# Performance work log

Hardware: AMD Instinct MI355X
Metric: run time of the kernel (lower is better)

The kernel has to match this reference:

```python
import jax, jax.numpy as jnp
import numpy as np

K = 20  # rec list length

def _isin(a, b, bmask=None):
    # membership of each element of a in (masked) b; a,b are small [K] int arrays
    eq = a[:, None] == b[None, :]
    if bmask is not None:
        eq = eq & bmask[None, :]
    return eq.any(axis=1)

def _compact(vals, mask):
    # stable compaction of masked elements to the front, preserving order
    n = vals.shape[0]
    order = jnp.argsort(jnp.where(mask, jnp.arange(n), n))
    return vals[order], mask.sum()

def _fuse_one(top, mid, sim, probs, key):
    # greedy set-intersection fusion of three K-length rec lists (mirrors __fuse_rec_lists)
    m_tm = _isin(top, mid)
    m_ts = _isin(top, sim)
    m_ms = _isin(mid, sim)
    # faithful to the torch code's elementwise AND of masks over different lists
    mask_common = m_tm & m_ts & m_ms
    in_common_mid = _isin(mid, top, mask_common)
    mask_tm = m_tm & ~mask_common
    mask_ts = m_ts & ~mask_common
    mask_ms = m_ms & ~in_common_mid
    top_pool_m = ~mask_common & ~mask_tm & ~mask_ts
    mid_pool_m = ~in_common_mid & ~_isin(mid, top, mask_tm) & ~mask_ms
    sim_pool_m = (~_isin(sim, top, mask_common) & ~_isin(sim, top, mask_ts)
                  & ~_isin(sim, mid, mask_ms))
    det_vals = jnp.concatenate([top, top, top, mid])          # [4K]
    det_mask = jnp.concatenate([mask_common, mask_tm, mask_ts, mask_ms])
    det, n_det = _compact(det_vals, det_mask)
    pools, counts = jax.vmap(_compact)(
        jnp.stack([top, mid, sim]),
        jnp.stack([top_pool_m, mid_pool_m, sim_pool_m]))      # [3,K], [3]
    logp = jnp.log(probs)

    def step(carry, t):
        ptr, key = carry
        key, sub = jax.random.split(key)
        avail = ptr < counts
        idx = jax.random.categorical(sub, jnp.where(avail, logp, -jnp.inf))
        sampled = pools[idx, jnp.minimum(ptr[idx], K - 1)]
        use_det = t < n_det
        val = jnp.where(use_det, det[t], sampled)
        ptr = ptr.at[idx].add(jnp.where(use_det, 0, 1))
        return (ptr, key), val

    _, out = jax.lax.scan(step, (jnp.zeros(3, jnp.int32), key), jnp.arange(K))
    return out

def setup_inputs() -> dict:
    key = jax.random.key(0)
    ks = jax.random.split(key, 9)
    B, p_dim, latent = 2048, 64, 128
    n_users, n_items = 2000, 20000
    n_top, n_mid = 2000, 5000
    rng = np.random.default_rng(0)
    perm = rng.permutation(n_items)
    return {
        "X": jax.random.normal(ks[0], (B, p_dim), jnp.float32),
        "W_sp": jax.random.normal(ks[1], (p_dim, latent), jnp.float32) * 0.1,
        "W_sd": jax.random.normal(ks[2], (latent, n_top), jnp.float32) * 0.1,
        "W_mp": jax.random.normal(ks[3], (p_dim, latent), jnp.float32) * 0.1,
        "W_md": jax.random.normal(ks[4], (latent, n_mid), jnp.float32) * 0.1,
        "W_mapper": jax.random.normal(ks[5], (p_dim, 3), jnp.float32) * 0.1,
        "user_ratings": jax.random.uniform(ks[6], (n_users, n_items), jnp.float32),
        "user_personalities": jax.random.normal(ks[7], (n_users, p_dim), jnp.float32),
        "top_map": jnp.asarray(perm[:n_top], jnp.int32),
        "mid_map": jnp.asarray(perm[n_top:n_top + n_mid], jnp.int32),
    }

def reference(X, W_sp, W_sd, W_mp, W_md, W_mapper, user_ratings,
              user_personalities, top_map, mid_map):
    B = X.shape[0]
    n_items = user_ratings.shape[1]
    # small decoder path: prior -> dec -> scatter into full item space
    top_sub = (X @ W_sp) @ W_sd                                  # [B, n_top]
    top_full = jnp.zeros((B, n_items), X.dtype).at[:, top_map].set(top_sub)
    mid_sub = (X @ W_mp) @ W_md                                  # [B, n_mid]
    mid_full = jnp.zeros((B, n_items), X.dtype).at[:, mid_map].set(mid_sub)
    # personality-similarity recommendations
    sim_scores = (X @ user_personalities.T) @ user_ratings       # [B, n_items]
    top_idx = jax.lax.top_k(top_full, K)[1].astype(jnp.int32)
    mid_idx = jax.lax.top_k(mid_full, K)[1].astype(jnp.int32)
    sim_idx = jax.lax.top_k(sim_scores, K)[1].astype(jnp.int32)
    probs = jax.nn.softmax(X @ W_mapper, axis=-1)                # [B, 3]
    keys = jax.random.split(jax.random.key(42), B)
    out = jax.vmap(_fuse_one)(top_idx, mid_idx, sim_idx, probs, keys)
    return out.astype(jnp.float32)                               # [B, K]
```

## Files before the change

kernel.cpp:

```cpp
#include <hip/hip_runtime.h>
#include <stdint.h>
#include <math.h>

#define KK 20
#define RNG_PARTITIONABLE 1


__device__ __forceinline__ void tf2x32(uint32_t k0, uint32_t k1,
                                       uint32_t c0, uint32_t c1,
                                       uint32_t& o0, uint32_t& o1) {
  const uint32_t ks2 = k0 ^ k1 ^ 0x1BD11BDAu;
  uint32_t x0 = c0 + k0, x1 = c1 + k1;
#define ROTL32(x,d) (((x) << (d)) | ((x) >> (32 - (d))))
#define R4(ra,rb,rc,rd) \
  x0 += x1; x1 = ROTL32(x1, ra); x1 ^= x0; \
  x0 += x1; x1 = ROTL32(x1, rb); x1 ^= x0; \
  x0 += x1; x1 = ROTL32(x1, rc); x1 ^= x0; \
  x0 += x1; x1 = ROTL32(x1, rd); x1 ^= x0;
  R4(13,15,26,6);  x0 += k1;  x1 += ks2 + 1u;
  R4(17,29,16,24); x0 += ks2; x1 += k0 + 2u;
  R4(13,15,26,6);  x0 += k0;  x1 += k1 + 3u;
  R4(17,29,16,24); x0 += k1;  x1 += ks2 + 4u;
  R4(13,15,26,6);  x0 += ks2; x1 += k0 + 5u;
  o0 = x0; o1 = x1;
#undef R4
#undef ROTL32
}

__device__ __forceinline__ float u01_from_bits(uint32_t b) {
  float f = __uint_as_float((b >> 9) | 0x3f800000u) - 1.0f;
  return (f == 0.0f) ? 1.17549435e-38f : f;
}

#define BK 32

__global__ __launch_bounds__(256) void gemm_nn_k(
    const float* __restrict__ A, int lda,
    const float* __restrict__ Bg, int ldb,
    float* __restrict__ C, int ldc,
    int M, int N, int K, int kc) {
  __shared__ __align__(16) float As[BK][64 + 4];
  __shared__ __align__(16) float Bs[BK][128 + 4];
  const int tid = threadIdx.x;
  const int row0 = blockIdx.y * 64;
  const int col0 = blockIdx.x * 128;
  const int tr = tid >> 4, tc = tid & 15;
  const int kc_eff = (kc > 0) ? kc : K;

  const int a_ar0 = tid >> 3,        a_ac0 = (tid & 7) << 2;
  const int a_ar1 = (tid + 256) >> 3, a_ac1 = ((tid + 256) & 7) << 2;
  int b_br[4], b_bc[4];
#pragma unroll
  for (int i = 0; i < 4; ++i) { int s = tid + i * 256; b_br[i] = s >> 5; b_bc[i] = (s & 31) << 2; }

  float4 pa0, pa1, pb[4];
  auto load_tile = [&](int k0) {
    {
      int gr = row0 + a_ar0, gc = k0 + a_ac0;
      float4 v = make_float4(0.f, 0.f, 0.f, 0.f);
      if (gr < M) {
        if (gc + 3 < K) v = *(const float4*)(A + (size_t)gr * lda + gc);
        else {
          float t0 = (gc     < K) ? A[(size_t)gr * lda + gc]     : 0.f;
          float t1 = (gc + 1 < K) ? A[(size_t)gr * lda + gc + 1] : 0.f;
          float t2 = (gc + 2 < K) ? A[(size_t)gr * lda + gc + 2] : 0.f;
          float t3 = (gc + 3 < K) ? A[(size_t)gr * lda + gc + 3] : 0.f;
          v = make_float4(t0, t1, t2, t3);
        }
      }
      pa0 = v;
    }
    {
      int gr = row0 + a_ar1, gc = k0 + a_ac1;
      float4 v = make_float4(0.f, 0.f, 0.f, 0.f);
      if (gr < M) {
        if (gc + 3 < K) v = *(const float4*)(A + (size_t)gr * lda + gc);
        else {
          float t0 = (gc     < K) ? A[(size_t)gr * lda + gc]     : 0.f;
          float t1 = (gc + 1 < K) ? A[(size_t)gr * lda + gc + 1] : 0.f;
          float t2 = (gc + 2 < K) ? A[(size_t)gr * lda + gc + 2] : 0.f;
          float t3 = (gc + 3 < K) ? A[(size_t)gr * lda + gc + 3] : 0.f;
          v = make_float4(t0, t1, t2, t3);
        }
      }
      pa1 = v;
    }
#pragma unroll
    for (int i = 0; i < 4; ++i) {
      int gk = k0 + b_br[i], gc = col0 + b_bc[i];
      float4 v = make_float4(0.f, 0.f, 0.f, 0.f);
      if (gk < K) {
        if (gc + 3 < N) v = *(const float4*)(Bg + (size_t)gk * ldb + gc);
        else {
          float t0 = (gc     < N) ? Bg[(size_t)gk * ldb + gc]     : 0.f;
          float t1 = (gc + 1 < N) ? Bg[(size_t)gk * ldb + gc + 1] : 0.f;
          float t2 = (gc + 2 < N) ? Bg[(size_t)gk * ldb + gc + 2] : 0.f;
          float t3 = (gc + 3 < N) ? Bg[(size_t)gk * ldb + gc + 3] : 0.f;
          v = make_float4(t0, t1, t2, t3);
        }
      }
      pb[i] = v;
    }
  };

  float accM[4][8];
#pragma unroll
  for (int i = 0; i < 4; ++i)
#pragma unroll
    for (int j = 0; j < 8; ++j) accM[i][j] = 0.f;

  for (int c0 = 0; c0 < K; c0 += kc_eff) {
    const int kend = (c0 + kc_eff < K) ? (c0 + kc_eff) : K;
    float acc[4][8];
#pragma unroll
    for (int i = 0; i < 4; ++i)
#pragma unroll
      for (int j = 0; j < 8; ++j) acc[i][j] = 0.f;

    load_tile(c0);
    for (int k0 = c0; k0 < kend; k0 += BK) {
      As[a_ac0 + 0][a_ar0] = pa0.x; As[a_ac0 + 1][a_ar0] = pa0.y;
      As[a_ac0 + 2][a_ar0] = pa0.z; As[a_ac0 + 3][a_ar0] = pa0.w;
      As[a_ac1 + 0][a_ar1] = pa1.x; As[a_ac1 + 1][a_ar1] = pa1.y;
      As[a_ac1 + 2][a_ar1] = pa1.z; As[a_ac1 + 3][a_ar1] = pa1.w;
#pragma unroll
      for (int i = 0; i < 4; ++i) *(float4*)&Bs[b_br[i]][b_bc[i]] = pb[i];
      __syncthreads();
      if (k0 + BK < kend) load_tile(k0 + BK);
      const int klim = (kend - k0 < BK) ? (kend - k0) : BK;
      for (int kk = 0; kk < klim; ++kk) {
        float4 av = *(const float4*)&As[kk][tr << 2];
        float4 b0 = *(const float4*)&Bs[kk][tc << 2];
        float4 b1 = *(const float4*)&Bs[kk][64 + (tc << 2)];
        float a[4] = {av.x, av.y, av.z, av.w};
        float b[8] = {b0.x, b0.y, b0.z, b0.w, b1.x, b1.y, b1.z, b1.w};
#pragma unroll
        for (int i = 0; i < 4; ++i)
#pragma unroll
          for (int j = 0; j < 8; ++j)
            acc[i][j] = __fadd_rn(acc[i][j], __fmul_rn(a[i], b[j]));
      }
      __syncthreads();
    }
#pragma unroll
    for (int i = 0; i < 4; ++i)
#pragma unroll
      for (int j = 0; j < 8; ++j) accM[i][j] = __fadd_rn(accM[i][j], acc[i][j]);
  }
#pragma unroll
  for (int i = 0; i < 4; ++i) {
    int gr = row0 + (tr << 2) + i;
    if (gr >= M) continue;
#pragma unroll
    for (int j = 0; j < 8; ++j) {
      int gc = col0 + ((j < 4) ? (tc << 2) + j : 64 + (tc << 2) + (j - 4));
      if (gc < N) C[(size_t)gr * ldc + gc] = accM[i][j];
    }
  }
}

__global__ __launch_bounds__(256) void gemm_nt_k(
    const float* __restrict__ A, int lda,
    const float* __restrict__ Bg, int ldb,
    float* __restrict__ C, int ldc,
    int M, int N, int K) {
  __shared__ __align__(16) float As[16][128 + 4];
  __shared__ __align__(16) float Bs[16][128 + 4];
  const int tid = threadIdx.x;
  const int row0 = blockIdx.y * 128;
  const int col0 = blockIdx.x * 128;
  const int tr = tid >> 4, tc = tid & 15;
  float acc[8][8];
#pragma unroll
  for (int i = 0; i < 8; ++i)
#pragma unroll
    for (int j = 0; j < 8; ++j) acc[i][j] = 0.f;

  for (int k0 = 0; k0 < K; k0 += 16) {
#pragma unroll
    for (int i = 0; i < 2; ++i) {
      int s = tid + i * 256;
      int ar = s >> 2, ac = (s & 3) << 2;
      int gr = row0 + ar, gc = k0 + ac;
      float4 v = make_float4(0.f, 0.f, 0.f, 0.f);
      if (gr < M) {
        if (gc + 3 < K) v = *(const float4*)(A + (size_t)gr * lda + gc);
        else {
          float t0 = (gc     < K) ? A[(size_t)gr * lda + gc]     : 0.f;
          float t1 = (gc + 1 < K) ? A[(size_t)gr * lda + gc + 1] : 0.f;
          float t2 = (gc + 2 < K) ? A[(size_t)gr * lda + gc + 2] : 0.f;
          float t3 = (gc + 3 < K) ? A[(size_t)gr * lda + gc + 3] : 0.f;
          v = make_float4(t0, t1, t2, t3);
        }
      }
      As[ac + 0][ar] = v.x; As[ac + 1][ar] = v.y;
      As[ac + 2][ar] = v.z; As[ac + 3][ar] = v.w;
    }
#pragma unroll
    for (int i = 0; i < 2; ++i) {
      int s = tid + i * 256;
      int nr = s >> 2, kcc = (s & 3) << 2;
      int gn = col0 + nr, gk = k0 + kcc;
      float4 v = make_float4(0.f, 0.f, 0.f, 0.f);
      if (gn < N) {
        if (gk + 3 < K) v = *(const float4*)(Bg + (size_t)gn * ldb + gk);
        else {
          float t0 = (gk     < K) ? Bg[(size_t)gn * ldb + gk]     : 0.f;
          float t1 = (gk + 1 < K) ? Bg[(size_t)gn * ldb + gk + 1] : 0.f;
          float t2 = (gk + 2 < K) ? Bg[(size_t)gn * ldb + gk + 2] : 0.f;
          float t3 = (gk + 3 < K) ? Bg[(size_t)gn * ldb + gk + 3] : 0.f;
          v = make_float4(t0, t1, t2, t3);
        }
      }
      Bs[kcc + 0][nr] = v.x; Bs[kcc + 1][nr] = v.y;
      Bs[kcc + 2][nr] = v.z; Bs[kcc + 3][nr] = v.w;
    }
    __syncthreads();
#pragma unroll
    for (int kk = 0; kk < 16; ++kk) {
      float4 a0 = *(const float4*)&As[kk][tr * 8];
      float4 a1 = *(const float4*)&As[kk][tr * 8 + 4];
      float4 b0 = *(const float4*)&Bs[kk][tc * 8];
      float4 b1 = *(const float4*)&Bs[kk][tc * 8 + 4];
      float a[8] = {a0.x, a0.y, a0.z, a0.w, a1.x, a1.y, a1.z, a1.w};
      float b[8] = {b0.x, b0.y, b0.z, b0.w, b1.x, b1.y, b1.z, b1.w};
#pragma unroll
      for (int i = 0; i < 8; ++i)
#pragma unroll
        for (int j = 0; j < 8; ++j)
          acc[i][j] = __fadd_rn(acc[i][j], __fmul_rn(a[i], b[j]));
    }
    __syncthreads();
  }
#pragma unroll
  for (int i = 0; i < 8; ++i) {
    int gr = row0 + tr * 8 + i;
    if (gr >= M) continue;
#pragma unroll
    for (int j = 0; j < 8; ++j) {
      int gc = col0 + tc * 8 + j;
      if (gc < N) C[(size_t)gr * ldc + gc] = acc[i][j];
    }
  }
}

__device__ __forceinline__ void topk20_row(
    const float* __restrict__ row, int ncols, int col_off,
    const int* __restrict__ map,
    float* __restrict__ SV, int* __restrict__ SI, int merge,
    float (*shv)[KK], int (*shi)[KK], float* ov, int* oi) {
  const int t = threadIdx.x;
  float lv[KK]; int li[KK];
#pragma unroll
  for (int i = 0; i < KK; ++i) { lv[i] = -INFINITY; li[i] = 0x7fffffff; }
  for (int c = t; c < ncols; c += 256) {
    float v = row[c];
    if (v > lv[KK - 1]) {
      float cv = v; int ci = c;
#pragma unroll
      for (int i = 0; i < KK; ++i) {
        bool sw = cv > lv[i];
        float tv = lv[i]; int ti = li[i];
        lv[i] = sw ? cv : tv; li[i] = sw ? ci : ti;
        cv = sw ? tv : cv;    ci = sw ? ti : ci;
      }
    }
  }
#pragma unroll
  for (int i = 0; i < KK; ++i) { shv[t][i] = lv[i]; shi[t][i] = li[i]; }
  __syncthreads();
  if (t < 64) {
    int hp0 = 0, hp1 = 0, hp2 = 0, hp3 = 0;
    for (int round = 0; round < KK; ++round) {
      int base = t * 4;
      float v0 = (hp0 < KK) ? shv[base + 0][hp0] : -INFINITY;
      int   i0 = (hp0 < KK) ? shi[base + 0][hp0] : 0x7fffffff;
      float v1 = (hp1 < KK) ? shv[base + 1][hp1] : -INFINITY;
      int   i1 = (hp1 < KK) ? shi[base + 1][hp1] : 0x7fffffff;
      float v2 = (hp2 < KK) ? shv[base + 2][hp2] : -INFINITY;
      int   i2 = (hp2 < KK) ? shi[base + 2][hp2] : 0x7fffffff;
      float v3 = (hp3 < KK) ? shv[base + 3][hp3] : -INFINITY;
      int   i3 = (hp3 < KK) ? shi[base + 3][hp3] : 0x7fffffff;
      float bv = v0; int bi = i0; int bq = 0;
      if (v1 > bv || (v1 == bv && i1 < bi)) { bv = v1; bi = i1; bq = 1; }
      if (v2 > bv || (v2 == bv && i2 < bi)) { bv = v2; bi = i2; bq = 2; }
      if (v3 > bv || (v3 == bv && i3 < bi)) { bv = v3; bi = i3; bq = 3; }
      float cv = bv; int ci = bi; int cl = t; int cq = bq;
#pragma unroll
      for (int s2 = 1; s2 < 64; s2 <<= 1) {
        float vx = __shfl_xor(cv, s2);
        int   ix = __shfl_xor(ci, s2);
        int   lx = __shfl_xor(cl, s2);
        int   qx = __shfl_xor(cq, s2);
        if (vx > cv || (vx == cv && ix < ci)) { cv = vx; ci = ix; cl = lx; cq = qx; }
      }
      if (t == 0) { ov[round] = cv; oi[round] = ci; }
      if (cl == t) { hp0 += (cq == 0); hp1 += (cq == 1); hp2 += (cq == 2); hp3 += (cq == 3); }
    }
    if (t == 0) {
      if (!merge) {
        for (int i = 0; i < KK; ++i) {
          SV[i] = ov[i];
          SI[i] = map ? map[oi[i]] : (oi[i] + col_off);
        }
      } else {
        float mv[KK]; int mi[KK];
        int a = 0, b = 0;
        for (int i = 0; i < KK; ++i) {
          float va = SV[a]; int ia = SI[a];
          float vb = ov[b]; int ib = oi[b] + col_off;
          bool ta = (va > vb) || (va == vb && ia < ib);
          if (ta) { mv[i] = va; mi[i] = ia; ++a; }
          else    { mv[i] = vb; mi[i] = ib; ++b; }
        }
        for (int i = 0; i < KK; ++i) { SV[i] = mv[i]; SI[i] = mi[i]; }
      }
    }
  }
}

__global__ __launch_bounds__(256) void topk20_k(
    const float* __restrict__ mat, int ld, int ncols, int col_off,
    const int* __restrict__ map,
    float* __restrict__ sval, int* __restrict__ sidx, int merge) {
  __shared__ float shv[256][KK];
  __shared__ int   shi[256][KK];
  __shared__ float ov[KK];
  __shared__ int   oi[KK];
  const int r = blockIdx.x;
  topk20_row(mat + (size_t)r * ld, ncols, col_off, map,
             sval + (size_t)r * KK, sidx + (size_t)r * KK, merge, shv, shi, ov, oi);
}

__global__ __launch_bounds__(256) void topk20_dual_k(
    const float* __restrict__ m0, int nc0, const int* __restrict__ map0,
    float* __restrict__ sv0, int* __restrict__ si0,
    const float* __restrict__ m1, int nc1, const int* __restrict__ map1,
    float* __restrict__ sv1, int* __restrict__ si1) {
  __shared__ float shv[256][KK];
  __shared__ int   shi[256][KK];
  __shared__ float ov[KK];
  __shared__ int   oi[KK];
  const int r = blockIdx.x;
  if (blockIdx.y == 0)
    topk20_row(m0 + (size_t)r * nc0, nc0, 0, map0,
               sv0 + (size_t)r * KK, si0 + (size_t)r * KK, 0, shv, shi, ov, oi);
  else
    topk20_row(m1 + (size_t)r * nc1, nc1, 0, map1,
               sv1 + (size_t)r * KK, si1 + (size_t)r * KK, 0, shv, shi, ov, oi);
}

__global__ __launch_bounds__(256) void fuse_k(
    const float* __restrict__ X, const float* __restrict__ Wmap,
    const int* __restrict__ siT, const int* __restrict__ siM,
    const int* __restrict__ siS, float* __restrict__ out, int B) {
  int r = blockIdx.x * blockDim.x + threadIdx.x;
  if (r >= B) return;
  int top[KK], mid[KK], sim[KK];
  for (int i = 0; i < KK; ++i) {
    top[i] = siT[(size_t)r * KK + i];
    mid[i] = siM[(size_t)r * KK + i];
    sim[i] = siS[(size_t)r * KK + i];
  }
  float z0 = 0.f, z1 = 0.f, z2 = 0.f;
  for (int k = 0; k < 64; ++k) {
    float x = X[(size_t)r * 64 + k];
    z0 = __fadd_rn(z0, __fmul_rn(x, Wmap[k * 3 + 0]));
    z1 = __fadd_rn(z1, __fmul_rn(x, Wmap[k * 3 + 1]));
    z2 = __fadd_rn(z2, __fmul_rn(x, Wmap[k * 3 + 2]));
  }
  float zm = fmaxf(z0, fmaxf(z1, z2));
  float e0 = expf(z0 - zm), e1 = expf(z1 - zm), e2 = expf(z2 - zm);
  float s = __fadd_rn(__fadd_rn(e0, e1), e2);
  float logp[3] = { logf(__fdiv_rn(e0, s)), logf(__fdiv_rn(e1, s)), logf(__fdiv_rn(e2, s)) };
  bool m_tm[KK], m_ts[KK], m_ms[KK], maskC[KK], inCmid[KK], mTM[KK], mTS[KK], mMS[KK];
  for (int i = 0; i < KK; ++i) {
    bool a = false, b = false, c = false;
    for (int j = 0; j < KK; ++j) {
      a |= (top[i] == mid[j]);
      b |= (top[i] == sim[j]);
      c |= (mid[i] == sim[j]);
    }
    m_tm[i] = a; m_ts[i] = b; m_ms[i] = c;
  }
  for (int i = 0; i < KK; ++i) maskC[i] = m_tm[i] && m_ts[i] && m_ms[i];
  for (int i = 0; i < KK; ++i) {
    bool v = false;
    for (int j = 0; j < KK; ++j) v |= (mid[i] == top[j]) && maskC[j];
    inCmid[i] = v;
  }
  for (int i = 0; i < KK; ++i) {
    mTM[i] = m_tm[i] && !maskC[i];
    mTS[i] = m_ts[i] && !maskC[i];
    mMS[i] = m_ms[i] && !inCmid[i];
  }
  bool poolT[KK], poolM[KK], poolS[KK];
  for (int i = 0; i < KK; ++i) poolT[i] = !maskC[i] && !mTM[i] && !mTS[i];
  for (int i = 0; i < KK; ++i) {
    bool v = false;
    for (int j = 0; j < KK; ++j) v |= (mid[i] == top[j]) && mTM[j];
    poolM[i] = !inCmid[i] && !v && !mMS[i];
  }
  for (int i = 0; i < KK; ++i) {
    bool v1 = false, v2 = false, v3 = false;
    for (int j = 0; j < KK; ++j) {
      v1 |= (sim[i] == top[j]) && maskC[j];
      v2 |= (sim[i] == top[j]) && mTS[j];
      v3 |= (sim[i] == mid[j]) && mMS[j];
    }
    poolS[i] = !v1 && !v2 && !v3;
  }
  int det[KK]; int ndet = 0;
  for (int i = 0; i < KK; ++i) if (maskC[i]) { if (ndet < KK) det[ndet] = top[i]; ndet++; }
  for (int i = 0; i < KK; ++i) if (mTM[i])  { if (ndet < KK) det[ndet] = top[i]; ndet++; }
  for (int i = 0; i < KK; ++i) if (mTS[i])  { if (ndet < KK) det[ndet] = top[i]; ndet++; }
  for (int i = 0; i < KK; ++i) if (mMS[i])  { if (ndet < KK) det[ndet] = mid[i]; ndet++; }
  int pool[3][KK]; int cnt[3];
  {
    int c = 0;
    for (int i = 0; i < KK; ++i) if (poolT[i]) pool[0][c++] = top[i];
    cnt[0] = c;
    for (int i = 0; i < KK; ++i) if (!poolT[i]) pool[0][c++] = top[i];
  }
  {
    int c = 0;
    for (int i = 0; i < KK; ++i) if (poolM[i]) pool[1][c++] = mid[i];
    cnt[1] = c;
    for (int i = 0; i < KK; ++i) if (!poolM[i]) pool[1][c++] = mid[i];
  }
  {
    int c = 0;
    for (int i = 0; i < KK; ++i) if (poolS[i]) pool[2][c++] = sim[i];
    cnt[2] = c;
    for (int i = 0; i < KK; ++i) if (!poolS[i]) pool[2][c++] = sim[i];
  }
  uint32_t k0, k1;
#if RNG_PARTITIONABLE
  { uint32_t a, b; tf2x32(0u, 42u, 0u, (uint32_t)r, a, b); k0 = a; k1 = b; }
#else
  {
    if (r < 1024) {
      uint32_t x0, x1, y0, y1;
      tf2x32(0u, 42u, (uint32_t)(2 * r),     (uint32_t)(2048 + 2 * r),     x0, x1);
      tf2x32(0u, 42u, (uint32_t)(2 * r + 1), (uint32_t)(2048 + 2 * r + 1), y0, y1);
      k0 = x0; k1 = y0;
    } else {
      int j = 2 * r - 2048;
      uint32_t x0, x1, y0, y1;
      tf2x32(0u, 42u, (uint32_t)j,       (uint32_t)(2048 + j),     x0, x1);
      tf2x32(0u, 42u, (uint32_t)(j + 1), (uint32_t)(2048 + j + 1), y0, y1);
      k0 = x1; k1 = y1;
    }
  }
#endif
  int ptr0 = 0, ptr1 = 0, ptr2 = 0;
  for (int t = 0; t < KK; ++t) {
    uint32_t nk0, nk1, sb0, sb1;
#if RNG_PARTITIONABLE
    tf2x32(k0, k1, 0u, 0u, nk0, nk1);
    tf2x32(k0, k1, 0u, 1u, sb0, sb1);
#else
    { uint32_t p0x, p0y, p1x, p1y;
      tf2x32(k0, k1, 0u, 2u, p0x, p0y);
      tf2x32(k0, k1, 1u, 3u, p1x, p1y);
      nk0 = p0x; nk1 = p1x; sb0 = p0y; sb1 = p1y; }
#endif
    k0 = nk0; k1 = nk1;
    float g[3];
#if RNG_PARTITIONABLE
    for (int i = 0; i < 3; ++i) {
      uint32_t a, b; tf2x32(sb0, sb1, 0u, (uint32_t)i, a, b);
      float u = u01_from_bits(a ^ b);
      g[i] = -logf(-logf(u));
    }
#else
    { uint32_t q0x, q0y, q1x, q1y;
      tf2x32(sb0, sb1, 0u, 2u, q0x, q0y);
      tf2x32(sb0, sb1, 1u, 0u, q1x, q1y);
      uint32_t bits[3] = { q0x, q1x, q0y };
      for (int i = 0; i < 3; ++i) {
        float u = u01_from_bits(bits[i]);
        g[i] = -logf(-logf(u));
      }
    }
#endif
    float s0 = (ptr0 < cnt[0]) ? g[0] + logp[0] : -INFINITY;
    float s1 = (ptr1 < cnt[1]) ? g[1] + logp[1] : -INFINITY;
    float s2 = (ptr2 < cnt[2]) ? g[2] + logp[2] : -INFINITY;
    int idx = 0; float best = s0;
    if (s1 > best) { best = s1; idx = 1; }
    if (s2 > best) { best = s2; idx = 2; }
    int p = (idx == 0) ? ptr0 : ((idx == 1) ? ptr1 : ptr2);
    int sampled = pool[idx][p < (KK - 1) ? p : (KK - 1)];
    int val = (t < ndet) ? det[t] : sampled;
    out[(size_t)r * KK + t] = (float)val;
    if (t >= ndet) { if (idx == 0) ++ptr0; else if (idx == 1) ++ptr1; else ++ptr2; }
  }
}

extern "C" void kernel_launch(void* const* d_in, const int* in_sizes, int n_in,
                              void* d_out, int out_size, void* d_ws, size_t ws_size,
                              hipStream_t stream) {
  const float* X    = (const float*)d_in[0];
  const float* Wsp  = (const float*)d_in[1];
  const float* Wsd  = (const float*)d_in[2];
  const float* Wmp  = (const float*)d_in[3];
  const float* Wmd  = (const float*)d_in[4];
  const float* Wmap = (const float*)d_in[5];
  const float* R    = (const float*)d_in[6];
  const float* U    = (const float*)d_in[7];
  const int* top_map = (const int*)d_in[8];
  const int* mid_map = (const int*)d_in[9];
  float* out = (float*)d_out;

  const int B = 2048, P_DIM = 64, LAT = 128;
  const int N_TOP = 2000, N_MID = 5000, N_USERS = 2000, N_ITEMS = 20000;
  const int KC_EIGEN = 320;
  (void)in_sizes; (void)n_in; (void)out_size;

  char* ws = (char*)d_ws;
  size_t off = 0;
  auto alloc = [&](size_t bytes) -> void* {
    off = (off + 255) & ~(size_t)255;
    void* p = ws + off; off += bytes; return p;
  };

  const size_t BIG_NEED = (size_t)B * (2 * LAT + N_USERS + N_TOP + N_MID + N_ITEMS + 6 * KK) * 4
                          + 16 * 256;
  const bool big = (ws_size >= BIG_NEED);

  dim3 blk(256);
  if (big) {
    float* Ht  = (float*)alloc((size_t)B * LAT * 4);
    float* Hm  = (float*)alloc((size_t)B * LAT * 4);
    float* Pm  = (float*)alloc((size_t)B * N_USERS * 4);
    float* CHt = (float*)alloc((size_t)B * N_TOP * 4);
    float* CHm = (float*)alloc((size_t)B * N_MID * 4);
    float* CHs = (float*)alloc((size_t)B * N_ITEMS * 4);
    float* svT = (float*)alloc((size_t)B * KK * 4);
    int*   siT = (int*)  alloc((size_t)B * KK * 4);
    float* svM = (float*)alloc((size_t)B * KK * 4);
    int*   siM = (int*)  alloc((size_t)B * KK * 4);
    float* svS = (float*)alloc((size_t)B * KK * 4);
    int*   siS = (int*)  alloc((size_t)B * KK * 4);

    gemm_nn_k<<<dim3(1, 32), blk, 0, stream>>>(X, P_DIM, Wsp, LAT, Ht, LAT, B, LAT, P_DIM, 0);
    gemm_nn_k<<<dim3(1, 32), blk, 0, stream>>>(X, P_DIM, Wmp, LAT, Hm, LAT, B, LAT, P_DIM, 0);
    gemm_nn_k<<<dim3(16, 32), blk, 0, stream>>>(Ht, LAT, Wsd, N_TOP, CHt, N_TOP, B, N_TOP, LAT, 0);
    gemm_nn_k<<<dim3(40, 32), blk, 0, stream>>>(Hm, LAT, Wmd, N_MID, CHm, N_MID, B, N_MID, LAT, 0);
    topk20_dual_k<<<dim3(B, 2), blk, 0, stream>>>(CHt, N_TOP, top_map, svT, siT,
                                                  CHm, N_MID, mid_map, svM, siM);
    gemm_nt_k<<<dim3(16, 16), blk, 0, stream>>>(X, P_DIM, U, P_DIM, Pm, N_USERS, B, N_USERS, P_DIM);
    gemm_nn_k<<<dim3(157, 32), blk, 0, stream>>>(Pm, N_USERS, R, N_ITEMS,
                                                 CHs, N_ITEMS, B, N_ITEMS, N_USERS, KC_EIGEN);
    topk20_k<<<dim3(B), blk, 0, stream>>>(CHs, N_ITEMS, N_ITEMS, 0, nullptr, svS, siS, 0);
    fuse_k<<<dim3(B / 256), blk, 0, stream>>>(X, Wmap, siT, siM, siS, out, B);
  } else {
    const int CHUNK = 5000, N_CHUNKS = 4;
    float* H   = (float*)alloc((size_t)B * LAT * 4);
    float* Pm  = (float*)alloc((size_t)B * N_USERS * 4);
    float* CH  = (float*)alloc((size_t)B * CHUNK * 4);
    float* svT = (float*)alloc((size_t)B * KK * 4);
    int*   siT = (int*)  alloc((size_t)B * KK * 4);
    float* svM = (float*)alloc((size_t)B * KK * 4);
    int*   siM = (int*)  alloc((size_t)B * KK * 4);
    float* svS = (float*)alloc((size_t)B * KK * 4);
    int*   siS = (int*)  alloc((size_t)B * KK * 4);

    gemm_nn_k<<<dim3(1, 32), blk, 0, stream>>>(X, P_DIM, Wsp, LAT, H, LAT, B, LAT, P_DIM, 0);
    gemm_nn_k<<<dim3(16, 32), blk, 0, stream>>>(H, LAT, Wsd, N_TOP, CH, N_TOP, B, N_TOP, LAT, 0);
    topk20_k<<<dim3(B), blk, 0, stream>>>(CH, N_TOP, N_TOP, 0, top_map, svT, siT, 0);
    gemm_nn_k<<<dim3(1, 32), blk, 0, stream>>>(X, P_DIM, Wmp, LAT, H, LAT, B, LAT, P_DIM, 0);
    gemm_nn_k<<<dim3(40, 32), blk, 0, stream>>>(H, LAT, Wmd, N_MID, CH, N_MID, B, N_MID, LAT, 0);
    topk20_k<<<dim3(B), blk, 0, stream>>>(CH, N_MID, N_MID, 0, mid_map, svM, siM, 0);
    gemm_nt_k<<<dim3(16, 16), blk, 0, stream>>>(X, P_DIM, U, P_DIM, Pm, N_USERS, B, N_USERS, P_DIM);
    for (int c = 0; c < N_CHUNKS; ++c) {
      gemm_nn_k<<<dim3(40, 32), blk, 0, stream>>>(Pm, N_USERS, R + (size_t)c * CHUNK, N_ITEMS,
                                                  CH, CHUNK, B, CHUNK, N_USERS, KC_EIGEN);
      topk20_k<<<dim3(B), blk, 0, stream>>>(CH, CHUNK, CHUNK, c * CHUNK, nullptr, svS, siS, c ? 1 : 0);
    }
    fuse_k<<<dim3(B / 256), blk, 0, stream>>>(X, Wmap, siT, siM, siS, out, B);
  }
}
```

Measured before the change: 3.669 ms.

## Double-buffer LDS in GEMM, merge prior GEMMs, chunk big similarity GEMM

Rewrites the NN GEMM to keep two LDS buffers with a K tile of 16, so the next tile is loaded into registers and stored to the spare buffer while the current one is computed. This removes one barrier per tile. The two small prior GEMMs are merged into one launch that picks its weight matrix from blockIdx.z. The big Pm@R GEMM is split into four column-chunk launches of 5000 items, which adds launch overhead and gives smaller grids, possibly with better cache locality on R.

After: 3.494 ms. 1.05x faster.

```diff
diff --git a/kernel.cpp b/kernel.cpp
--- a/kernel.cpp
+++ b/kernel.cpp
@@ -32,31 +32,29 @@
   return (f == 0.0f) ? 1.17549435e-38f : f;
 }
 
-#define BK 32
-
-__global__ __launch_bounds__(256) void gemm_nn_k(
+#define GK 16
+
+__device__ __forceinline__ void gemm_nn_body(
     const float* __restrict__ A, int lda,
     const float* __restrict__ Bg, int ldb,
     float* __restrict__ C, int ldc,
-    int M, int N, int K, int kc) {
-  __shared__ __align__(16) float As[BK][64 + 4];
-  __shared__ __align__(16) float Bs[BK][128 + 4];
+    int M, int N, int K, int kc,
+    float (*As)[68], float (*Bs)[132]) {
   const int tid = threadIdx.x;
   const int row0 = blockIdx.y * 64;
   const int col0 = blockIdx.x * 128;
   const int tr = tid >> 4, tc = tid & 15;
   const int kc_eff = (kc > 0) ? kc : K;
 
-  const int a_ar0 = tid >> 3,        a_ac0 = (tid & 7) << 2;
-  const int a_ar1 = (tid + 256) >> 3, a_ac1 = ((tid + 256) & 7) << 2;
-  int b_br[4], b_bc[4];
-#pragma unroll
-  for (int i = 0; i < 4; ++i) { int s = tid + i * 256; b_br[i] = s >> 5; b_bc[i] = (s & 31) << 2; }
-
-  float4 pa0, pa1, pb[4];
-  auto load_tile = [&](int k0) {
+  const int a_ar = tid >> 2, a_ac = (tid & 3) << 2;
+  int b_br[2], b_bc[2];
+#pragma unroll
+  for (int i = 0; i < 2; ++i) { int s = tid + i * 256; b_br[i] = s >> 5; b_bc[i] = (s & 31) << 2; }
+
+  float4 pa, pb[2];
+  auto load_regs = [&](int k0) {
     {
-      int gr = row0 + a_ar0, gc = k0 + a_ac0;
+      int gr = row0 + a_ar, gc = k0 + a_ac;
       float4 v = make_float4(0.f, 0.f, 0.f, 0.f);
       if (gr < M) {
         if (gc + 3 < K) v = *(const float4*)(A + (size_t)gr * lda + gc);
@@ -68,25 +66,10 @@
           v = make_float4(t0, t1, t2, t3);
         }
       }
-      pa0 = v;
-    }
-    {
-      int gr = row0 + a_ar1, gc = k0 + a_ac1;
-      float4 v = make_float4(0.f, 0.f, 0.f, 0.f);
-      if (gr < M) {
-        if (gc + 3 < K) v = *(const float4*)(A + (size_t)gr * lda + gc);
-        else {
-          float t0 = (gc     < K) ? A[(size_t)gr * lda + gc]     : 0.f;
-          float t1 = (gc + 1 < K) ? A[(size_t)gr * lda + gc + 1] : 0.f;
-          float t2 = (gc + 2 < K) ? A[(size_t)gr * lda + gc + 2] : 0.f;
-          float t3 = (gc + 3 < K) ? A[(size_t)gr * lda + gc + 3] : 0.f;
-          v = make_float4(t0, t1, t2, t3);
-        }
-      }
-      pa1 = v;
-    }
-#pragma unroll
-    for (int i = 0; i < 4; ++i) {
+      pa = v;
+    }
+#pragma unroll
+    for (int i = 0; i < 2; ++i) {
       int gk = k0 + b_br[i], gc = col0 + b_bc[i];
       float4 v = make_float4(0.f, 0.f, 0.f, 0.f);
       if (gk < K) {
@@ -102,6 +85,14 @@
       pb[i] = v;
     }
   };
+  auto store_lds = [&](int buf) {
+    float (*Ab)[68] = As + buf * GK;
+    float (*Bb)[132] = Bs + buf * GK;
+    Ab[a_ac + 0][a_ar] = pa.x; Ab[a_ac + 1][a_ar] = pa.y;
+    Ab[a_ac + 2][a_ar] = pa.z; Ab[a_ac + 3][a_ar] = pa.w;
+#pragma unroll
+    for (int i = 0; i < 2; ++i) *(float4*)&Bb[b_br[i]][b_bc[i]] = pb[i];
+  };
 
   float accM[4][8];
 #pragma unroll
@@ -111,27 +102,28 @@
 
   for (int c0 = 0; c0 < K; c0 += kc_eff) {
     const int kend = (c0 + kc_eff < K) ? (c0 + kc_eff) : K;
+    const int ntile = (kend - c0 + GK - 1) / GK;
     float acc[4][8];
 #pragma unroll
     for (int i = 0; i < 4; ++i)
 #pragma unroll
       for (int j = 0; j < 8; ++j) acc[i][j] = 0.f;
 
-    load_tile(c0);
-    for (int k0 = c0; k0 < kend; k0 += BK) {
-      As[a_ac0 + 0][a_ar0] = pa0.x; As[a_ac0 + 1][a_ar0] = pa0.y;
-      As[a_ac0 + 2][a_ar0] = pa0.z; As[a_ac0 + 3][a_ar0] = pa0.w;
-      As[a_ac1 + 0][a_ar1] = pa1.x; As[a_ac1 + 1][a_ar1] = pa1.y;
-      As[a_ac1 + 2][a_ar1] = pa1.z; As[a_ac1 + 3][a_ar1] = pa1.w;
-#pragma unroll
-      for (int i = 0; i < 4; ++i) *(float4*)&Bs[b_br[i]][b_bc[i]] = pb[i];
-      __syncthreads();
-      if (k0 + BK < kend) load_tile(k0 + BK);
-      const int klim = (kend - k0 < BK) ? (kend - k0) : BK;
+    load_regs(c0);
+    store_lds(0);
+    __syncthreads();
+    int cur = 0;
+    for (int t = 0; t < ntile; ++t) {
+      const int k0 = c0 + t * GK;
+      const bool has_next = (t + 1 < ntile);
+      if (has_next) load_regs(k0 + GK);
+      float (*Ab)[68] = As + cur * GK;
+      float (*Bb)[132] = Bs + cur * GK;
+      const int klim = (kend - k0 < GK) ? (kend - k0) : GK;
       for (int kk = 0; kk < klim; ++kk) {
-        float4 av = *(const float4*)&As[kk][tr << 2];
-        float4 b0 = *(const float4*)&Bs[kk][tc << 2];
-        float4 b1 = *(const float4*)&Bs[kk][64 + (tc << 2)];
+        float4 av = *(const float4*)&Ab[kk][tr << 2];
+        float4 b0 = *(const float4*)&Bb[kk][tc << 2];
+        float4 b1 = *(const float4*)&Bb[kk][64 + (tc << 2)];
         float a[4] = {av.x, av.y, av.z, av.w};
         float b[8] = {b0.x, b0.y, b0.z, b0.w, b1.x, b1.y, b1.z, b1.w};
 #pragma unroll
@@ -140,8 +132,13 @@
           for (int j = 0; j < 8; ++j)
             acc[i][j] = __fadd_rn(acc[i][j], __fmul_rn(a[i], b[j]));
       }
-      __syncthreads();
-    }
+      if (has_next) {
+        store_lds(1 - cur);
+        __syncthreads();
+        cur ^= 1;
+      }
+    }
+    __syncthreads();
 #pragma unroll
     for (int i = 0; i < 4; ++i)
 #pragma unroll
@@ -157,6 +154,29 @@
       if (gc < N) C[(size_t)gr * ldc + gc] = accM[i][j];
     }
   }
+}
+
+__global__ __launch_bounds__(256) void gemm_nn_k(
+    const float* __restrict__ A, int lda,
+    const float* __restrict__ Bg, int ldb,
+    float* __restrict__ C, int ldc,
+    int M, int N, int K, int kc) {
+  __shared__ __align__(16) float As[2 * GK][68];
+  __shared__ __align__(16) float Bs[2 * GK][132];
+  gemm_nn_body(A, lda, Bg, ldb, C, ldc, M, N, K, kc, As, Bs);
+}
+
+__global__ __launch_bounds__(256) void gemm_prior_k(
+    const float* __restrict__ X,
+    const float* __restrict__ Wsp, const float* __restrict__ Wmp,
+    float* __restrict__ Ht, float* __restrict__ Hm,
+    int B, int P, int L) {
+  __shared__ __align__(16) float As[2 * GK][68];
+  __shared__ __align__(16) float Bs[2 * GK][132];
+  if (blockIdx.z == 0)
+    gemm_nn_body(X, P, Wsp, L, Ht, L, B, L, P, 0, As, Bs);
+  else
+    gemm_nn_body(X, P, Wmp, L, Hm, L, B, L, P, 0, As, Bs);
 }
 
 __global__ __launch_bounds__(256) void gemm_nt_k(
@@ -515,6 +535,7 @@
 
   const int B = 2048, P_DIM = 64, LAT = 128;
   const int N_TOP = 2000, N_MID = 5000, N_USERS = 2000, N_ITEMS = 20000;
+  const int CHUNK = 5000, N_CHUNKS = 4;
   const int KC_EIGEN = 320;
   (void)in_sizes; (void)n_in; (void)out_size;
 
@@ -544,19 +565,20 @@
     float* svS = (float*)alloc((size_t)B * KK * 4);
     int*   siS = (int*)  alloc((size_t)B * KK * 4);
 
-    gemm_nn_k<<<dim3(1, 32), blk, 0, stream>>>(X, P_DIM, Wsp, LAT, Ht, LAT, B, LAT, P_DIM, 0);
-    gemm_nn_k<<<dim3(1, 32), blk, 0, stream>>>(X, P_DIM, Wmp, LAT, Hm, LAT, B, LAT, P_DIM, 0);
+    gemm_prior_k<<<dim3(1, 32, 2), blk, 0, stream>>>(X, Wsp, Wmp, Ht, Hm, B, P_DIM, LAT);
     gemm_nn_k<<<dim3(16, 32), blk, 0, stream>>>(Ht, LAT, Wsd, N_TOP, CHt, N_TOP, B, N_TOP, LAT, 0);
     gemm_nn_k<<<dim3(40, 32), blk, 0, stream>>>(Hm, LAT, Wmd, N_MID, CHm, N_MID, B, N_MID, LAT, 0);
     topk20_dual_k<<<dim3(B, 2), blk, 0, stream>>>(CHt, N_TOP, top_map, svT, siT,
                                                   CHm, N_MID, mid_map, svM, siM);
     gemm_nt_k<<<dim3(16, 16), blk, 0, stream>>>(X, P_DIM, U, P_DIM, Pm, N_USERS, B, N_USERS, P_DIM);
-    gemm_nn_k<<<dim3(157, 32), blk, 0, stream>>>(Pm, N_USERS, R, N_ITEMS,
-                                                 CHs, N_ITEMS, B, N_ITEMS, N_USERS, KC_EIGEN);
+    for (int c = 0; c < N_CHUNKS; ++c) {
+      gemm_nn_k<<<dim3(40, 32), blk, 0, stream>>>(Pm, N_USERS, R + (size_t)c * CHUNK, N_ITEMS,
+                                                  CHs + (size_t)c * CHUNK, N_ITEMS,
+                                                  B, CHUNK, N_USERS, KC_EIGEN);
+    }
     topk20_k<<<dim3(B), blk, 0, stream>>>(CHs, N_ITEMS, N_ITEMS, 0, nullptr, svS, siS, 0);
     fuse_k<<<dim3(B / 256), blk, 0, stream>>>(X, Wmap, siT, siM, siS, out, B);
   } else {
-    const int CHUNK = 5000, N_CHUNKS = 4;
     float* H   = (float*)alloc((size_t)B * LAT * 4);
     float* Pm  = (float*)alloc((size_t)B * N_USERS * 4);
     float* CH  = (float*)alloc((size_t)B * CHUNK * 4);
```
